# Kernel tuning notes

Measured on AMD Instinct MI355X. Metric: run time of the kernel, lower is better.

## Reference

```python
import jax, jax.numpy as jnp
import numpy as np

NEG_INF = -1e9  # mask fill; every row has >=1 valid key so softmax is well-defined


def setup_inputs() -> dict:
    B, L, E, A = 4096, 200, 128, 128
    key = jax.random.key(0)
    ks = jax.random.split(key, 8)
    scale = 0.05
    return {
        "query": jax.random.normal(ks[0], (B, E), dtype=jnp.float32),
        "keys": jax.random.normal(ks[1], (B, L, E), dtype=jnp.float32),
        "keys_length": jax.random.randint(ks[2], (B,), 1, L + 1, dtype=jnp.int64),
        "pos_emb": jax.random.normal(ks[3], (L, E), dtype=jnp.float32) * scale,
        "W1": jax.random.normal(ks[4], (4 * E, A), dtype=jnp.float32) * scale,
        "b1": jnp.zeros((A,), dtype=jnp.float32),
        "W2": jax.random.normal(ks[5], (A, A), dtype=jnp.float32) * scale,
        "b2": jnp.zeros((A,), dtype=jnp.float32),
        "W3": jax.random.normal(ks[6], (A, 1), dtype=jnp.float32) * scale,
        "b3": jnp.zeros((1,), dtype=jnp.float32),
    }


def reference(query, keys, keys_length, pos_emb, W1, b1, W2, b2, W3, b3):
    B, L, E = keys.shape
    # add position embedding (positions are simply arange(L) for every batch row)
    keys_p = keys + pos_emb[None, :, :]                      # (B, L, E)
    q = jnp.broadcast_to(query[:, None, :], (B, L, E))       # (B, L, E)
    # DIN attention input: [q, k, q-k, q*k] -> (B, L, 4E)
    att_in = jnp.concatenate([q, keys_p, q - keys_p, q * keys_p], axis=-1)
    h = jax.nn.relu(att_in @ W1 + b1)                        # (B, L, A)
    h = jax.nn.relu(h @ W2 + b2)                             # (B, L, A)
    scores = (h @ W3 + b3)[..., 0]                           # (B, L)
    valid = jnp.arange(L)[None, :] < keys_length[:, None]    # (B, L) bool
    scores = jnp.where(valid, scores, NEG_INF)
    weights = jax.nn.softmax(scores, axis=-1)                # (B, L)
    out = jnp.einsum("bl,ble->be", weights, keys_p)          # (B, E)
    return out
```

## Files before the change

### kernel.cpp

```cpp
#include <hip/hip_runtime.h>
#include <hip/hip_bf16.h>


typedef __attribute__((ext_vector_type(8))) short short8;
typedef __attribute__((ext_vector_type(4))) float f32x4;

__device__ __forceinline__ float bf2f(short s) {
    return __uint_as_float(((unsigned)(unsigned short)s) << 16);
}
__device__ __forceinline__ short f2bf(float f) {
    unsigned u = __float_as_uint(f);
    u = (u + 0x7fff + ((u >> 16) & 1)) >> 16;
    return (short)u;
}

__global__ void prep_frag(const float* __restrict__ W1, const float* __restrict__ W2,
                          short* __restrict__ F1, short* __restrict__ F2) {
    int idx = blockIdx.x * 256 + threadIdx.x;
    if (idx < 4096) {
        int lane = idx & 63, n = (idx >> 6) & 7, kb = idx >> 9;
        int q = lane >> 4, l15 = lane & 15;
        int sp = kb >> 1, half = kb & 1;
        int col = n * 16 + l15;
        short8 v;
        #pragma unroll
        for (int j = 0; j < 8; ++j) {
            int k = 32 * sp + 8 * q + j;
            float x = half ? W1[(384 + k) * 128 + col]
                           : W1[(128 + k) * 128 + col] - W1[(256 + k) * 128 + col];
            v[j] = f2bf(x);
        }
        *(short8*)(F1 + idx * 8) = v;
    } else if (idx < 6144) {
        int i2 = idx - 4096;
        int lane = i2 & 63, n = (i2 >> 6) & 7, s2 = i2 >> 9;
        int q = lane >> 4, l15 = lane & 15;
        int col = n * 16 + l15;
        short8 v;
        #pragma unroll
        for (int j = 0; j < 8; ++j)
            v[j] = f2bf(W2[(32 * s2 + 8 * q + j) * 128 + col]);
        *(short8*)(F2 + i2 * 8) = v;
    }
}

__global__ void prep_qw(const float* __restrict__ query, const float* __restrict__ W1,
                        const float* __restrict__ b1, float* __restrict__ qw) {
    __shared__ float qsh[128];
    const int b = blockIdx.x, t = threadIdx.x;
    qsh[t] = query[b * 128 + t];
    __syncthreads();
    float acc = b1[t];
    #pragma unroll 4
    for (int k = 0; k < 128; ++k)
        acc += qsh[k] * (W1[k * 128 + t] + W1[(256 + k) * 128 + t]);
    qw[b * 128 + t] = acc;
}

#define HSTR 136

__launch_bounds__(256, 2)
__global__ void din_main(const float* __restrict__ query, const float* __restrict__ keys,
                         const int* __restrict__ klen, const float* __restrict__ pos,
                         const float* __restrict__ b2g, const float* __restrict__ w3g,
                         const float* __restrict__ qw, const short* __restrict__ F1,
                         const short* __restrict__ F2, float* __restrict__ out) {
    __shared__ alignas(16) short h1buf[16 * 16 * HSTR];
    __shared__ float qv[128];
    __shared__ float s_lds[208];
    __shared__ float w_lds[208];
    __shared__ float part[512];
    __shared__ float red[8];

    const int t = threadIdx.x;
    const int b = blockIdx.x;
    const int w = t >> 6;
    const int lane = t & 63;
    const int quad = lane >> 4;
    const int l15 = lane & 15;

    const int len = klen[b];
    const int T = (len + 15) >> 4;
    const int cnt = (T > w) ? ((T - w + 3) >> 2) : 0;

    if (t < 128) qv[t] = query[b * 128 + t];
    __syncthreads();

    f32x4 acc[4][8];
    #pragma unroll
    for (int i = 0; i < 4; ++i)
        #pragma unroll
        for (int n = 0; n < 8; ++n) acc[i][n] = (f32x4){0.f, 0.f, 0.f, 0.f};

    if (cnt > 0) {
        for (int sp = 0; sp < 4; ++sp) {
            float4 qa = *(const float4*)(qv + 32 * sp + 8 * quad);
            float4 qb = *(const float4*)(qv + 32 * sp + 8 * quad + 4);
            short8 bf[8];
            #pragma unroll
            for (int n = 0; n < 8; ++n)
                bf[n] = *(const short8*)(F1 + (((2 * sp) * 8 + n) * 64 + lane) * 8);
            short8 af[4];
            #pragma unroll
            for (int i = 0; i < 4; ++i) {
                if (i < cnt) {
                    int row = (w + 4 * i) * 16 + l15;
                    short8 a;
                    if (row < 200) {
                        const float* kr = keys + ((long)b * 200 + row) * 128 + 32 * sp + 8 * quad;
                        const float* pr = pos + (long)row * 128 + 32 * sp + 8 * quad;
                        float4 k0 = *(const float4*)kr, k1 = *(const float4*)(kr + 4);
                        float4 p0 = *(const float4*)pr, p1 = *(const float4*)(pr + 4);
                        a[0] = f2bf(k0.x + p0.x); a[1] = f2bf(k0.y + p0.y);
                        a[2] = f2bf(k0.z + p0.z); a[3] = f2bf(k0.w + p0.w);
                        a[4] = f2bf(k1.x + p1.x); a[5] = f2bf(k1.y + p1.y);
                        a[6] = f2bf(k1.z + p1.z); a[7] = f2bf(k1.w + p1.w);
                    } else {
                        #pragma unroll
                        for (int j = 0; j < 8; ++j) a[j] = 0;
                    }
                    af[i] = a;
                    #pragma unroll
                    for (int n = 0; n < 8; ++n)
                        acc[i][n] = __builtin_amdgcn_mfma_f32_16x16x32_bf16(a, bf[n], acc[i][n], 0, 0, 0);
                }
            }
            #pragma unroll
            for (int n = 0; n < 8; ++n)
                bf[n] = *(const short8*)(F1 + (((2 * sp + 1) * 8 + n) * 64 + lane) * 8);
            #pragma unroll
            for (int i = 0; i < 4; ++i) {
                if (i < cnt) {
                    short8 a;
                    a[0] = f2bf(bf2f(af[i][0]) * qa.x); a[1] = f2bf(bf2f(af[i][1]) * qa.y);
                    a[2] = f2bf(bf2f(af[i][2]) * qa.z); a[3] = f2bf(bf2f(af[i][3]) * qa.w);
                    a[4] = f2bf(bf2f(af[i][4]) * qb.x); a[5] = f2bf(bf2f(af[i][5]) * qb.y);
                    a[6] = f2bf(bf2f(af[i][6]) * qb.z); a[7] = f2bf(bf2f(af[i][7]) * qb.w);
                    #pragma unroll
                    for (int n = 0; n < 8; ++n)
                        acc[i][n] = __builtin_amdgcn_mfma_f32_16x16x32_bf16(a, bf[n], acc[i][n], 0, 0, 0);
                }
            }
        }

        {
            float qwn[8];
            #pragma unroll
            for (int n = 0; n < 8; ++n) qwn[n] = qw[b * 128 + n * 16 + l15];
            #pragma unroll
            for (int i = 0; i < 4; ++i) {
                if (i < cnt) {
                    #pragma unroll
                    for (int n = 0; n < 8; ++n)
                        #pragma unroll
                        for (int r = 0; r < 4; ++r) {
                            float v = acc[i][n][r] + qwn[n];
                            h1buf[((w * 4 + i) * 16 + quad * 4 + r) * HSTR + n * 16 + l15] =
                                f2bf(v > 0.f ? v : 0.f);
                        }
                }
            }
        }

        #pragma unroll
        for (int i = 0; i < 4; ++i)
            #pragma unroll
            for (int n = 0; n < 8; ++n) acc[i][n] = (f32x4){0.f, 0.f, 0.f, 0.f};
        for (int s2 = 0; s2 < 4; ++s2) {
            short8 bf[8];
            #pragma unroll
            for (int n = 0; n < 8; ++n)
                bf[n] = *(const short8*)(F2 + ((s2 * 8 + n) * 64 + lane) * 8);
            #pragma unroll
            for (int i = 0; i < 4; ++i) {
                if (i < cnt) {
                    short8 a = *(const short8*)(h1buf + ((w * 4 + i) * 16 + l15) * HSTR + 32 * s2 + 8 * quad);
                    #pragma unroll
                    for (int n = 0; n < 8; ++n)
                        acc[i][n] = __builtin_amdgcn_mfma_f32_16x16x32_bf16(a, bf[n], acc[i][n], 0, 0, 0);
                }
            }
        }

        {
            float b2n[8], w3n[8];
            #pragma unroll
            for (int n = 0; n < 8; ++n) {
                b2n[n] = b2g[n * 16 + l15];
                w3n[n] = w3g[n * 16 + l15];
            }
            #pragma unroll
            for (int i = 0; i < 4; ++i) {
                if (i < cnt) {
                    float p[4] = {0.f, 0.f, 0.f, 0.f};
                    #pragma unroll
                    for (int n = 0; n < 8; ++n)
                        #pragma unroll
                        for (int r = 0; r < 4; ++r) {
                            float v = acc[i][n][r] + b2n[n];
                            p[r] += (v > 0.f ? v : 0.f) * w3n[n];
                        }
                    #pragma unroll
                    for (int off = 8; off >= 1; off >>= 1)
                        #pragma unroll
                        for (int r = 0; r < 4; ++r) p[r] += __shfl_xor(p[r], off, 64);
                    if (l15 == 0) {
                        #pragma unroll
                        for (int r = 0; r < 4; ++r)
                            s_lds[(w + 4 * i) * 16 + quad * 4 + r] = p[r];
                    }
                }
            }
        }
    }
    __syncthreads();

    float sv = (t < 208 && t < len) ? s_lds[t] : -1e9f;
    float m = sv;
    #pragma unroll
    for (int off = 32; off >= 1; off >>= 1) m = fmaxf(m, __shfl_xor(m, off, 64));
    if (lane == 0) red[w] = m;
    __syncthreads();
    m = fmaxf(fmaxf(red[0], red[1]), fmaxf(red[2], red[3]));
    float e = (t < 208 && t < len) ? expf(sv - m) : 0.f;
    float ssum = e;
    #pragma unroll
    for (int off = 32; off >= 1; off >>= 1) ssum += __shfl_xor(ssum, off, 64);
    if (lane == 0) red[4 + w] = ssum;
    __syncthreads();
    float S = red[4] + red[5] + red[6] + red[7];
    if (t < 208) w_lds[t] = e / S;
    __syncthreads();

    const int qt = t >> 6;
    const int e2h = t & 63;
    float ax = 0.f, ay = 0.f;
    const float2* kr = (const float2*)(keys + (long)b * 200 * 128);
    const float2* pr = (const float2*)pos;
    for (int l = qt; l < len; l += 4) {
        float wgt = w_lds[l];
        float2 kv = kr[l * 64 + e2h];
        float2 pv = pr[l * 64 + e2h];
        ax += wgt * (kv.x + pv.x);
        ay += wgt * (kv.y + pv.y);
    }
    part[qt * 128 + 2 * e2h]     = ax;
    part[qt * 128 + 2 * e2h + 1] = ay;
    __syncthreads();
    if (t < 128) {
        float o = part[t] + part[128 + t] + part[256 + t] + part[384 + t];
        out[b * 128 + t] = o;
    }
}

extern "C" void kernel_launch(void* const* d_in, const int* in_sizes, int n_in,
                              void* d_out, int out_size, void* d_ws, size_t ws_size,
                              hipStream_t stream) {
    const float* query = (const float*)d_in[0];
    const float* keys  = (const float*)d_in[1];
    const int*   klen  = (const int*)  d_in[2];
    const float* pos   = (const float*)d_in[3];
    const float* W1    = (const float*)d_in[4];
    const float* b1    = (const float*)d_in[5];
    const float* W2    = (const float*)d_in[6];
    const float* b2    = (const float*)d_in[7];
    const float* W3    = (const float*)d_in[8];
    float* out = (float*)d_out;

    char* ws = (char*)d_ws;
    float* qw = (float*)ws;
    short* F1 = (short*)(ws + 2097152);
    short* F2 = (short*)(ws + 2097152 + 65536);

    prep_frag<<<24,   256, 0, stream>>>(W1, W2, F1, F2);
    prep_qw  <<<4096, 128, 0, stream>>>(query, W1, b1, qw);
    din_main <<<4096, 256, 0, stream>>>(query, keys, klen, pos, b2, W3, qw,
                                        F1, F2, out);
}
```

Baseline: 716.0 us.

## Process row tiles one at a time to cut registers and LDS, raise occupancy

The MLP stage now loops over each warp's 16-row tiles one by one instead of holding four tiles of accumulators at once. This shrinks the accumulator register footprint and the h1 LDS buffer fourfold, so launch bounds can ask for three blocks per SIMD-group instead of two. The weighted-sum tail is also unrolled four ways with independent accumulators to expose more memory-level parallelism. In exchange, the F1/F2 weight fragments are reloaded for every tile instead of once per block, and there is less instruction-level parallelism within each tile.

```diff
diff --git a/kernel.cpp b/kernel.cpp
--- a/kernel.cpp
+++ b/kernel.cpp
@@ -59,13 +59,13 @@
 
 #define HSTR 136
 
-__launch_bounds__(256, 2)
+__launch_bounds__(256, 3)
 __global__ void din_main(const float* __restrict__ query, const float* __restrict__ keys,
                          const int* __restrict__ klen, const float* __restrict__ pos,
                          const float* __restrict__ b2g, const float* __restrict__ w3g,
                          const float* __restrict__ qw, const short* __restrict__ F1,
                          const short* __restrict__ F2, float* __restrict__ out) {
-    __shared__ alignas(16) short h1buf[16 * 16 * HSTR];
+    __shared__ alignas(16) short h1buf[4 * 16 * HSTR];
     __shared__ float qv[128];
     __shared__ float s_lds[208];
     __shared__ float w_lds[208];
@@ -86,130 +86,101 @@
     if (t < 128) qv[t] = query[b * 128 + t];
     __syncthreads();
 
-    f32x4 acc[4][8];
-    #pragma unroll
-    for (int i = 0; i < 4; ++i)
-        #pragma unroll
-        for (int n = 0; n < 8; ++n) acc[i][n] = (f32x4){0.f, 0.f, 0.f, 0.f};
-
-    if (cnt > 0) {
+    for (int c = 0; c < 4; ++c) {
+        if (c >= cnt) break;
+
+        const int tile = w + 4 * c;
+        const int row = tile * 16 + l15;
+
+        f32x4 acc[8];
+        #pragma unroll
+        for (int n = 0; n < 8; ++n) acc[n] = (f32x4){0.f, 0.f, 0.f, 0.f};
+
         for (int sp = 0; sp < 4; ++sp) {
-            float4 qa = *(const float4*)(qv + 32 * sp + 8 * quad);
-            float4 qb = *(const float4*)(qv + 32 * sp + 8 * quad + 4);
-            short8 bf[8];
-            #pragma unroll
-            for (int n = 0; n < 8; ++n)
-                bf[n] = *(const short8*)(F1 + (((2 * sp) * 8 + n) * 64 + lane) * 8);
-            short8 af[4];
-            #pragma unroll
-            for (int i = 0; i < 4; ++i) {
-                if (i < cnt) {
-                    int row = (w + 4 * i) * 16 + l15;
-                    short8 a;
-                    if (row < 200) {
-                        const float* kr = keys + ((long)b * 200 + row) * 128 + 32 * sp + 8 * quad;
-                        const float* pr = pos + (long)row * 128 + 32 * sp + 8 * quad;
-                        float4 k0 = *(const float4*)kr, k1 = *(const float4*)(kr + 4);
-                        float4 p0 = *(const float4*)pr, p1 = *(const float4*)(pr + 4);
-                        a[0] = f2bf(k0.x + p0.x); a[1] = f2bf(k0.y + p0.y);
-                        a[2] = f2bf(k0.z + p0.z); a[3] = f2bf(k0.w + p0.w);
-                        a[4] = f2bf(k1.x + p1.x); a[5] = f2bf(k1.y + p1.y);
-                        a[6] = f2bf(k1.z + p1.z); a[7] = f2bf(k1.w + p1.w);
-                    } else {
-                        #pragma unroll
-                        for (int j = 0; j < 8; ++j) a[j] = 0;
-                    }
-                    af[i] = a;
-                    #pragma unroll
-                    for (int n = 0; n < 8; ++n)
-                        acc[i][n] = __builtin_amdgcn_mfma_f32_16x16x32_bf16(a, bf[n], acc[i][n], 0, 0, 0);
-                }
-            }
-            #pragma unroll
-            for (int n = 0; n < 8; ++n)
-                bf[n] = *(const short8*)(F1 + (((2 * sp + 1) * 8 + n) * 64 + lane) * 8);
-            #pragma unroll
-            for (int i = 0; i < 4; ++i) {
-                if (i < cnt) {
-                    short8 a;
-                    a[0] = f2bf(bf2f(af[i][0]) * qa.x); a[1] = f2bf(bf2f(af[i][1]) * qa.y);
-                    a[2] = f2bf(bf2f(af[i][2]) * qa.z); a[3] = f2bf(bf2f(af[i][3]) * qa.w);
-                    a[4] = f2bf(bf2f(af[i][4]) * qb.x); a[5] = f2bf(bf2f(af[i][5]) * qb.y);
-                    a[6] = f2bf(bf2f(af[i][6]) * qb.z); a[7] = f2bf(bf2f(af[i][7]) * qb.w);
-                    #pragma unroll
-                    for (int n = 0; n < 8; ++n)
-                        acc[i][n] = __builtin_amdgcn_mfma_f32_16x16x32_bf16(a, bf[n], acc[i][n], 0, 0, 0);
-                }
-            }
-        }
-
-        {
-            float qwn[8];
-            #pragma unroll
-            for (int n = 0; n < 8; ++n) qwn[n] = qw[b * 128 + n * 16 + l15];
-            #pragma unroll
-            for (int i = 0; i < 4; ++i) {
-                if (i < cnt) {
-                    #pragma unroll
-                    for (int n = 0; n < 8; ++n)
-                        #pragma unroll
-                        for (int r = 0; r < 4; ++r) {
-                            float v = acc[i][n][r] + qwn[n];
-                            h1buf[((w * 4 + i) * 16 + quad * 4 + r) * HSTR + n * 16 + l15] =
-                                f2bf(v > 0.f ? v : 0.f);
-                        }
-                }
-            }
-        }
-
-        #pragma unroll
-        for (int i = 0; i < 4; ++i)
-            #pragma unroll
-            for (int n = 0; n < 8; ++n) acc[i][n] = (f32x4){0.f, 0.f, 0.f, 0.f};
+            short8 af;
+            #pragma unroll
+            for (int j = 0; j < 8; ++j) af[j] = 0;
+            if (row < 200) {
+                const float* kr = keys + ((long)b * 200 + row) * 128 + 32 * sp + 8 * quad;
+                const float* pr = pos + (long)row * 128 + 32 * sp + 8 * quad;
+                float4 k0 = *(const float4*)kr, k1 = *(const float4*)(kr + 4);
+                float4 p0 = *(const float4*)pr, p1 = *(const float4*)(pr + 4);
+                af[0] = f2bf(k0.x + p0.x); af[1] = f2bf(k0.y + p0.y);
+                af[2] = f2bf(k0.z + p0.z); af[3] = f2bf(k0.w + p0.w);
+                af[4] = f2bf(k1.x + p1.x); af[5] = f2bf(k1.y + p1.y);
+                af[6] = f2bf(k1.z + p1.z); af[7] = f2bf(k1.w + p1.w);
+            }
+            {
+                short8 bf[8];
+                #pragma unroll
+                for (int n = 0; n < 8; ++n)
+                    bf[n] = *(const short8*)(F1 + (((2 * sp) * 8 + n) * 64 + lane) * 8);
+                #pragma unroll
+                for (int n = 0; n < 8; ++n)
+                    acc[n] = __builtin_amdgcn_mfma_f32_16x16x32_bf16(af, bf[n], acc[n], 0, 0, 0);
+            }
+            {
+                float4 qa = *(const float4*)(qv + 32 * sp + 8 * quad);
+                float4 qb = *(const float4*)(qv + 32 * sp + 8 * quad + 4);
+                short8 aq;
+                aq[0] = f2bf(bf2f(af[0]) * qa.x); aq[1] = f2bf(bf2f(af[1]) * qa.y);
+                aq[2] = f2bf(bf2f(af[2]) * qa.z); aq[3] = f2bf(bf2f(af[3]) * qa.w);
+                aq[4] = f2bf(bf2f(af[4]) * qb.x); aq[5] = f2bf(bf2f(af[5]) * qb.y);
+                aq[6] = f2bf(bf2f(af[6]) * qb.z); aq[7] = f2bf(bf2f(af[7]) * qb.w);
+                short8 bf[8];
+                #pragma unroll
+                for (int n = 0; n < 8; ++n)
+                    bf[n] = *(const short8*)(F1 + (((2 * sp + 1) * 8 + n) * 64 + lane) * 8);
+                #pragma unroll
+                for (int n = 0; n < 8; ++n)
+                    acc[n] = __builtin_amdgcn_mfma_f32_16x16x32_bf16(aq, bf[n], acc[n], 0, 0, 0);
+            }
+        }
+
+        #pragma unroll
+        for (int n = 0; n < 8; ++n) {
+            float qwn = qw[b * 128 + n * 16 + l15];
+            #pragma unroll
+            for (int r = 0; r < 4; ++r) {
+                float v = acc[n][r] + qwn;
+                h1buf[(w * 16 + quad * 4 + r) * HSTR + n * 16 + l15] =
+                    f2bf(v > 0.f ? v : 0.f);
+            }
+        }
+
+        #pragma unroll
+        for (int n = 0; n < 8; ++n) acc[n] = (f32x4){0.f, 0.f, 0.f, 0.f};
         for (int s2 = 0; s2 < 4; ++s2) {
+            short8 a2 = *(const short8*)(h1buf + (w * 16 + l15) * HSTR + 32 * s2 + 8 * quad);
             short8 bf[8];
             #pragma unroll
             for (int n = 0; n < 8; ++n)
                 bf[n] = *(const short8*)(F2 + ((s2 * 8 + n) * 64 + lane) * 8);
             #pragma unroll
-            for (int i = 0; i < 4; ++i) {
-                if (i < cnt) {
-                    short8 a = *(const short8*)(h1buf + ((w * 4 + i) * 16 + l15) * HSTR + 32 * s2 + 8 * quad);
-                    #pragma unroll
-                    for (int n = 0; n < 8; ++n)
-                        acc[i][n] = __builtin_amdgcn_mfma_f32_16x16x32_bf16(a, bf[n], acc[i][n], 0, 0, 0);
+            for (int n = 0; n < 8; ++n)
+                acc[n] = __builtin_amdgcn_mfma_f32_16x16x32_bf16(a2, bf[n], acc[n], 0, 0, 0);
+        }
+
+        {
+            float p[4] = {0.f, 0.f, 0.f, 0.f};
+            #pragma unroll
+            for (int n = 0; n < 8; ++n) {
+                float b2n = b2g[n * 16 + l15];
+                float w3n = w3g[n * 16 + l15];
+                #pragma unroll
+                for (int r = 0; r < 4; ++r) {
+                    float v = acc[n][r] + b2n;
+                    p[r] += (v > 0.f ? v : 0.f) * w3n;
                 }
             }
-        }
-
-        {
-            float b2n[8], w3n[8];
-            #pragma unroll
-            for (int n = 0; n < 8; ++n) {
-                b2n[n] = b2g[n * 16 + l15];
-                w3n[n] = w3g[n * 16 + l15];
-            }
-            #pragma unroll
-            for (int i = 0; i < 4; ++i) {
-                if (i < cnt) {
-                    float p[4] = {0.f, 0.f, 0.f, 0.f};
-                    #pragma unroll
-                    for (int n = 0; n < 8; ++n)
-                        #pragma unroll
-                        for (int r = 0; r < 4; ++r) {
-                            float v = acc[i][n][r] + b2n[n];
-                            p[r] += (v > 0.f ? v : 0.f) * w3n[n];
-                        }
-                    #pragma unroll
-                    for (int off = 8; off >= 1; off >>= 1)
-                        #pragma unroll
-                        for (int r = 0; r < 4; ++r) p[r] += __shfl_xor(p[r], off, 64);
-                    if (l15 == 0) {
-                        #pragma unroll
-                        for (int r = 0; r < 4; ++r)
-                            s_lds[(w + 4 * i) * 16 + quad * 4 + r] = p[r];
-                    }
-                }
+            #pragma unroll
+            for (int off = 8; off >= 1; off >>= 1)
+                #pragma unroll
+                for (int r = 0; r < 4; ++r) p[r] += __shfl_xor(p[r], off, 64);
+            if (l15 == 0) {
+                #pragma unroll
+                for (int r = 0; r < 4; ++r)
+                    s_lds[tile * 16 + quad * 4 + r] = p[r];
             }
         }
     }
@@ -234,18 +205,31 @@
 
     const int qt = t >> 6;
     const int e2h = t & 63;
-    float ax = 0.f, ay = 0.f;
     const float2* kr = (const float2*)(keys + (long)b * 200 * 128);
     const float2* pr = (const float2*)pos;
-    for (int l = qt; l < len; l += 4) {
+    float ax0 = 0.f, ay0 = 0.f, ax1 = 0.f, ay1 = 0.f;
+    float ax2 = 0.f, ay2 = 0.f, ax3 = 0.f, ay3 = 0.f;
+    int l = qt;
+    for (; l + 12 < len; l += 16) {
+        float w0 = w_lds[l], w1 = w_lds[l + 4], w2 = w_lds[l + 8], w3 = w_lds[l + 12];
+        float2 k0 = kr[l * 64 + e2h],        p0 = pr[l * 64 + e2h];
+        float2 k1 = kr[(l + 4) * 64 + e2h],  p1 = pr[(l + 4) * 64 + e2h];
+        float2 k2 = kr[(l + 8) * 64 + e2h],  p2 = pr[(l + 8) * 64 + e2h];
+        float2 k3 = kr[(l + 12) * 64 + e2h], p3 = pr[(l + 12) * 64 + e2h];
+        ax0 += w0 * (k0.x + p0.x); ay0 += w0 * (k0.y + p0.y);
+        ax1 += w1 * (k1.x + p1.x); ay1 += w1 * (k1.y + p1.y);
+        ax2 += w2 * (k2.x + p2.x); ay2 += w2 * (k2.y + p2.y);
+        ax3 += w3 * (k3.x + p3.x); ay3 += w3 * (k3.y + p3.y);
+    }
+    for (; l < len; l += 4) {
         float wgt = w_lds[l];
         float2 kv = kr[l * 64 + e2h];
         float2 pv = pr[l * 64 + e2h];
-        ax += wgt * (kv.x + pv.x);
-        ay += wgt * (kv.y + pv.y);
-    }
-    part[qt * 128 + 2 * e2h]     = ax;
-    part[qt * 128 + 2 * e2h + 1] = ay;
+        ax0 += wgt * (kv.x + pv.x);
+        ay0 += wgt * (kv.y + pv.y);
+    }
+    part[qt * 128 + 2 * e2h]     = (ax0 + ax1) + (ax2 + ax3);
+    part[qt * 128 + 2 * e2h + 1] = (ay0 + ay1) + (ay2 + ay3);
     __syncthreads();
     if (t < 128) {
         float o = part[t] + part[128 + t] + part[256 + t] + part[384 + t];
```

Result: slower. 1.541 ms (+115.3%).
